# Kernel tuning notes

Measured on AMD Instinct MI355X. Metric: run time of the kernel, lower is better.

## Reference

```python
import jax, jax.numpy as jnp
from jax import lax
import numpy as np

H = 512      # hidden_size
L = 2        # num_layers
IN = 512     # input_size
LAT = 256    # latent_size
B = 256      # batch
S = 256      # seq_length


def setup_inputs() -> dict:
    key = jax.random.key(0)
    ks = jax.random.split(key, 12)
    sd = 0.05
    return {
        "latent": jax.random.normal(ks[0], (B, LAT), dtype=jnp.float32),
        "fc_w": jax.random.normal(ks[1], (H * L * 2, LAT), dtype=jnp.float32) * sd,
        "fc_b": jnp.zeros((H * L * 2,), dtype=jnp.float32),
        "map_w": jax.random.normal(ks[2], (IN, H * 2 * L), dtype=jnp.float32) * sd,
        "map_b": jnp.zeros((IN,), dtype=jnp.float32),
        "wih0": jax.random.normal(ks[3], (4 * H, IN), dtype=jnp.float32) * sd,
        "whh0": jax.random.normal(ks[4], (4 * H, H), dtype=jnp.float32) * sd,
        "bih0": jnp.zeros((4 * H,), dtype=jnp.float32),
        "bhh0": jnp.zeros((4 * H,), dtype=jnp.float32),
        "wih1": jax.random.normal(ks[5], (4 * H, H), dtype=jnp.float32) * sd,
        "whh1": jax.random.normal(ks[6], (4 * H, H), dtype=jnp.float32) * sd,
        "bih1": jnp.zeros((4 * H,), dtype=jnp.float32),
        "bhh1": jnp.zeros((4 * H,), dtype=jnp.float32),
        "seq_length": S,
    }


def _lstm_cell(x, h, c, wih, whh, bih, bhh):
    # torch.nn.LSTMCell gate ordering: i, f, g, o
    g = x @ wih.T + bih + h @ whh.T + bhh
    i, f, gg, o = jnp.split(g, 4, axis=-1)
    c2 = jax.nn.sigmoid(f) * c + jax.nn.sigmoid(i) * jnp.tanh(gg)
    h2 = jax.nn.sigmoid(o) * jnp.tanh(c2)
    return h2, c2


def reference(latent, fc_w, fc_b, map_w, map_b,
              wih0, whh0, bih0, bhh0, wih1, whh1, bih1, bhh1, seq_length):
    bsz = latent.shape[0]
    hid = wih0.shape[0] // 4
    nl = 2
    # dec_hidden = tanh(fc(latent)) -> view(num_layers, B, 2H) -> chunk into (h, c)
    dec = jnp.tanh(latent @ fc_w.T + fc_b)            # (B, 2*L*H)
    dec = dec.reshape(nl, bsz, 2 * hid)               # row-major reinterpret, as torch .view
    h0, c0 = dec[..., :hid], dec[..., hid:]           # each (L, B, H)
    wih = (wih0, wih1); whh = (whh0, whh1)
    bih = (bih0, bih1); bhh = (bhh0, bhh1)

    def step(carry, _):
        h, c = carry
        # cat((h,c), -1).view(B, -1) -- faithful raw reshape across (layer, batch)
        fc_in = jnp.concatenate([h, c], axis=-1).reshape(bsz, -1)  # (B, 2*L*H)
        out = jax.nn.sigmoid(fc_in @ map_w.T + map_b)              # (B, IN)
        x = out
        hs, cs = [], []
        for l in range(nl):
            h2, c2 = _lstm_cell(x, h[l], c[l], wih[l], whh[l], bih[l], bhh[l])
            hs.append(h2); cs.append(c2)
            x = h2
        hn = jnp.tanh(jnp.stack(hs))   # activation_rnn
        cn = jnp.tanh(jnp.stack(cs))   # activation_fc
        return (hn, cn), out

    _, outs = lax.scan(step, (h0, c0), None, length=int(seq_length))
    return outs  # (S, B, IN)
```

## Files before the change

### kernel.cpp

```cpp
#include <hip/hip_runtime.h>

#define SEQ 256

#define WL0     0u
#define WL1     2097152u
#define FCT     4194304u
#define OFF_FC  4718592u
#define OFF_XM  5767168u
#define OFF_X0  5898240u
#define OFF_ARR 6029312u

#define S_AS0 0
#define S_WS0 2304
#define S_AS1 4608
#define S_WS1 6912
#define S_RED 9216
#define S_GS  17664
#define S_TOT 18720

__device__ __forceinline__ float sigf(float x){ return 1.0f/(1.0f + __expf(-x)); }
__device__ __forceinline__ float tanhf_(float x){
  float cx = fminf(fmaxf(x, -15.f), 15.f);
  float e = __expf(2.f*cx);
  return (e-1.f)/(e+1.f);
}

__global__ __launch_bounds__(256) void tr_kernel(const float* __restrict__ src,
                                                 float* __restrict__ dst, int R, int C){
  int i = blockIdx.x*256 + threadIdx.x;
  if (i < R*C){ int r = i / C, c = i - r*C; dst[(size_t)c*R + r] = src[i]; }
}

__global__ __launch_bounds__(256) void wprep(const float* __restrict__ wih0,
                                             const float* __restrict__ whh0,
                                             const float* __restrict__ wih1,
                                             const float* __restrict__ whh1,
                                             float* __restrict__ ws){
  const unsigned idx = blockIdx.x*256u + threadIdx.x;
  const unsigned layer = idx >> 21, rem = idx & 2097151u;
  const unsigned c = rem >> 10, k = rem & 1023u;
  const unsigned j = c >> 2, g = c & 3u;
  const float* wih = layer ? wih1 : wih0;
  const float* whh = layer ? whh1 : whh0;
  const float v = (k < 512u) ? wih[(g*512u + j)*512u + k] : whh[(g*512u + j)*512u + (k - 512u)];
  ws[(layer ? WL1 : WL0) + rem] = v;
}

__global__ __launch_bounds__(256) void init2(const float* __restrict__ latent,
                                             const float* __restrict__ fc_b,
                                             float* __restrict__ ws){
  __shared__ float ls[256];
  const int b = blockIdx.x, tid = threadIdx.x;
  if (tid < 32){
    __hip_atomic_store((unsigned*)(ws + OFF_ARR) + b*32 + tid, 0u,
                       __ATOMIC_RELAXED, __HIP_MEMORY_SCOPE_AGENT);
    __hip_atomic_store((unsigned*)(ws + OFF_ARR) + (b+256)*32 + tid, 0u,
                       __ATOMIC_RELAXED, __HIP_MEMORY_SCOPE_AGENT);
  }
  ls[tid] = latent[b*256 + tid];
  __syncthreads();
  const float* fT = ws + FCT;
  for (int nc = 0; nc < 8; ++nc){
    const int n = nc*256 + tid;
    float acc = fc_b[n];
    for (int k = 0; k < 256; ++k) acc += ls[k] * fT[k*2048 + n];
    const float v = tanhf_(acc);
    const unsigned f = (unsigned)b*2048u + (unsigned)n;
    const unsigned l = f >> 18, p = (f >> 10) & 255u, q = f & 1023u;
    ws[OFF_FC + (l*128u + (p>>1))*2048u + (p&1u)*1024u + q] = v;
  }
}

__device__ __forceinline__ void gsync(unsigned* arr, unsigned epoch, int tid, int blk){
  __syncthreads();
  if (tid == 0)
    __hip_atomic_store(arr + (unsigned)blk*32u, epoch,
                       __ATOMIC_RELEASE, __HIP_MEMORY_SCOPE_AGENT);
  if (tid < 64){
    unsigned m;
    do {
      m = 0xFFFFFFFFu;
      #pragma unroll
      for (int q = 0; q < 8; ++q){
        const unsigned v = __hip_atomic_load(arr + (unsigned)(tid + 64*q)*32u,
                                             __ATOMIC_RELAXED, __HIP_MEMORY_SCOPE_AGENT);
        m = v < m ? v : m;
      }
      if (m < epoch) __builtin_amdgcn_s_sleep(2);
    } while (!__all(m >= epoch));
  }
  __syncthreads();
  if (tid == 0) __builtin_amdgcn_fence(__ATOMIC_ACQUIRE, "agent");
  __syncthreads();
}

__device__ __forceinline__ void fma8x4(float acc[8][4], const float4 A0, const float4 A1,
                                       const float4 W0){
  const float a_[8] = {A0.x,A0.y,A0.z,A0.w,A1.x,A1.y,A1.z,A1.w};
  const float w_[4] = {W0.x,W0.y,W0.z,W0.w};
  #pragma unroll
  for (int i=0;i<8;++i)
    #pragma unroll
    for (int j=0;j<4;++j) acc[i][j] = __builtin_fmaf(a_[i], w_[j], acc[i][j]);
}

__device__ __forceinline__ void map_phase(float* sm, const float* __restrict__ FCc,
    const float* __restrict__ map_w, const float* __restrict__ map_b,
    float* __restrict__ XM, float* __restrict__ outp_t, int tid, int r0, int cb)
{
  const int rg = tid & 3;
  const int ng = (tid >> 2) & 1;
  const int kg = tid >> 3;
  const int n0 = cb * 8;
  float acc[8][4];
  #pragma unroll
  for (int i=0;i<8;++i){
    #pragma unroll
    for (int j=0;j<4;++j) acc[i][j]=0.f;
  }
  float4 va[2]; float4 vw;

  auto LOADS = [&](int ch){
    #pragma unroll
    for (int it=0; it<2; ++it){
      const int e = tid + it*256, r = e>>4, kq = e&15;
      va[it] = *(const float4*)&FCc[(unsigned)(r0+r)*2048u + (unsigned)(ch*64 + kq*4)];
    }
    if (tid < 128){ const int n = tid>>4, kq = tid&15;
      vw = *(const float4*)&map_w[(unsigned)(n0+n)*2048u + (unsigned)(ch*64 + kq*4)]; }
  };
  auto STORES = [&](int buf){
    float* A_ = sm + (buf ? S_AS1 : S_AS0);
    float* W_ = sm + (buf ? S_WS1 : S_WS0);
    #pragma unroll
    for (int it=0; it<2; ++it){
      const int e = tid + it*256, r = e>>4, kq = e&15;
      const int col = r ^ ((kq&7)<<2);
      A_[(kq*4+0)*36 + col] = va[it].x;
      A_[(kq*4+1)*36 + col] = va[it].y;
      A_[(kq*4+2)*36 + col] = va[it].z;
      A_[(kq*4+3)*36 + col] = va[it].w;
    }
    if (tid < 128){ const int n = tid>>4, kq = tid&15;
      const int col = n ^ ((kq&7)<<2);
      W_[(kq*4+0)*36 + col] = vw.x;
      W_[(kq*4+1)*36 + col] = vw.y;
      W_[(kq*4+2)*36 + col] = vw.z;
      W_[(kq*4+3)*36 + col] = vw.w; }
  };
  auto COMPUTE = [&](int buf){
    const float* A_ = sm + (buf ? S_AS1 : S_AS0);
    const float* W_ = sm + (buf ? S_WS1 : S_WS0);
    #pragma unroll
    for (int u=0; u<2; ++u){
      const int k = kg*2 + u;
      const int phi = ((k>>2)&7)<<2;
      const int ca0 = (rg*8) ^ phi;
      const float4 a0 = *(const float4*)&A_[k*36 + ca0];
      const float4 a1 = *(const float4*)&A_[k*36 + (ca0^4)];
      const float4 w0 = *(const float4*)&W_[k*36 + ((ng*4) ^ phi)];
      fma8x4(acc, a0, a1, w0);
    }
  };

  LOADS(0); STORES(1);
  __syncthreads();
  #pragma unroll 1
  for (int ch = 0; ch < 32; ++ch){
    const int buf = (ch & 1) ^ 1;
    if (ch+1 < 32) LOADS(ch+1);
    COMPUTE(buf);
    if (ch+1 < 32) STORES(buf^1);
    __syncthreads();
  }
  float* red = sm + S_RED;
  #pragma unroll
  for (int i=0;i<8;++i){
    #pragma unroll
    for (int j=0;j<4;++j) red[tid*33 + i*4 + j] = acc[i][j];
  }
  __syncthreads();
  {
    const int r = tid >> 3, nl = tid & 7;
    float sum = 0.f;
    #pragma unroll
    for (int kk=0;kk<32;++kk)
      sum += red[((r>>3) + 4*(nl>>2) + 8*kk)*33 + (r&7)*4 + (nl&3)];
    const int n = n0 + nl;
    const float v = sigf(sum + map_b[n]);
    const unsigned off = (unsigned)(r0 + r)*512u + (unsigned)n;
    XM[off] = v;
    outp_t[off] = v;
  }
}

__device__ __forceinline__ void lstm_phase(float* sm, const int l,
    const float* __restrict__ WL, const float* __restrict__ xs,
    const float* __restrict__ FCc, float* __restrict__ FCn,
    float* __restrict__ X0, const float* __restrict__ bih, const float* __restrict__ bhh,
    int tid, int r0, int cb)
{
  const int rg = tid & 3;
  const int ng = (tid >> 2) & 7;
  const int kg = tid >> 5;
  const int c0 = cb * 32;
  float acc[8][4];
  #pragma unroll
  for (int i=0;i<8;++i){
    #pragma unroll
    for (int j=0;j<4;++j) acc[i][j]=0.f;
  }
  float4 va[2], vw4[2];

  auto LOADS = [&](int ch){
    if (ch < 8){
      #pragma unroll
      for (int it=0; it<2; ++it){
        const int e = tid + it*256, r = e>>4, kq = e&15;
        va[it] = *(const float4*)&xs[(unsigned)(r0+r)*512u + (unsigned)(ch*64 + kq*4)];
      }
    } else {
      #pragma unroll
      for (int it=0; it<2; ++it){
        const int e = tid + it*256, r = e>>4, kq = e&15;
        const int b = r0 + r;
        const unsigned q = (unsigned)((ch-8)*64 + kq*4);
        va[it] = *(const float4*)&FCc[(unsigned)((l<<7) + (b>>1))*2048u + (unsigned)(b&1)*1024u + q];
      }
    }
    #pragma unroll
    for (int it=0; it<2; ++it){
      const int e = tid + it*256, n = e>>4, kq = e&15;
      vw4[it] = *(const float4*)&WL[(unsigned)(c0+n)*1024u + (unsigned)(ch*64 + kq*4)];
    }
  };
  auto STORES = [&](int buf){
    float* A_ = sm + (buf ? S_AS1 : S_AS0);
    float* W_ = sm + (buf ? S_WS1 : S_WS0);
    #pragma unroll
    for (int it=0; it<2; ++it){
      const int e = tid + it*256, r = e>>4, kq = e&15;
      const int col = r ^ ((kq&7)<<2);
      A_[(kq*4+0)*36 + col] = va[it].x;
      A_[(kq*4+1)*36 + col] = va[it].y;
      A_[(kq*4+2)*36 + col] = va[it].z;
      A_[(kq*4+3)*36 + col] = va[it].w;
    }
    #pragma unroll
    for (int it=0; it<2; ++it){
      const int e = tid + it*256, n = e>>4, kq = e&15;
      const int col = n ^ ((kq&7)<<2);
      W_[(kq*4+0)*36 + col] = vw4[it].x;
      W_[(kq*4+1)*36 + col] = vw4[it].y;
      W_[(kq*4+2)*36 + col] = vw4[it].z;
      W_[(kq*4+3)*36 + col] = vw4[it].w;
    }
  };
  auto COMPUTE = [&](int buf){
    const float* A_ = sm + (buf ? S_AS1 : S_AS0);
    const float* W_ = sm + (buf ? S_WS1 : S_WS0);
    #pragma unroll
    for (int u=0; u<8; ++u){
      const int k = kg*8 + u;
      const int phi = ((k>>2)&7)<<2;
      const int ca0 = (rg*8) ^ phi;
      const float4 a0 = *(const float4*)&A_[k*36 + ca0];
      const float4 a1 = *(const float4*)&A_[k*36 + (ca0^4)];
      const float4 w0 = *(const float4*)&W_[k*36 + ((ng*4) ^ phi)];
      fma8x4(acc, a0, a1, w0);
    }
  };

  LOADS(0); STORES(1);
  __syncthreads();
  #pragma unroll 1
  for (int ch = 0; ch < 16; ++ch){
    const int buf = (ch & 1) ^ 1;
    if (ch+1 < 16) LOADS(ch+1);
    COMPUTE(buf);
    if (ch+1 < 16) STORES(buf^1);
    __syncthreads();
  }

  float* red = sm + S_RED;
  float* gs  = sm + S_GS;
  #pragma unroll
  for (int i=0;i<8;++i){
    #pragma unroll
    for (int j=0;j<4;++j) red[tid*33 + i*4 + j] = acc[i][j];
  }
  __syncthreads();
  #pragma unroll
  for (int s=0;s<4;++s){
    const int o = tid + s*256;
    const int r = o >> 5, c = o & 31;
    float sum = 0.f;
    #pragma unroll
    for (int kk=0;kk<8;++kk)
      sum += red[((r>>3) + 4*(c>>2) + 32*kk)*33 + (r&7)*4 + (c&3)];
    gs[c*33 + r] = sum;
  }
  __syncthreads();
  const int r = tid & 31, j0 = tid >> 5;
  const int row = r0 + r;
  const unsigned srow = (unsigned)((l<<7) + (row>>1))*2048u + (unsigned)(row&1)*1024u;
  const int jg = cb*8 + j0;
  const float gi = gs[(j0*4+0)*33 + r] + bih[jg]       + bhh[jg];
  const float gf = gs[(j0*4+1)*33 + r] + bih[512+jg]   + bhh[512+jg];
  const float gg = gs[(j0*4+2)*33 + r] + bih[1024+jg]  + bhh[1024+jg];
  const float go = gs[(j0*4+3)*33 + r] + bih[1536+jg]  + bhh[1536+jg];
  const float cp = FCc[srow + 512u + (unsigned)jg];
  const float c2 = sigf(gf)*cp + sigf(gi)*tanhf_(gg);
  const float h2 = sigf(go)*tanhf_(c2);
  if (l == 0) X0[(unsigned)row*512u + (unsigned)jg] = h2;
  FCn[srow + (unsigned)jg]        = tanhf_(h2);
  FCn[srow + 512u + (unsigned)jg] = tanhf_(c2);
}

__launch_bounds__(256, 2)
__global__ void persist(const float* __restrict__ map_w, const float* __restrict__ map_b,
                        const float* __restrict__ bih0, const float* __restrict__ bhh0,
                        const float* __restrict__ bih1, const float* __restrict__ bhh1,
                        float* __restrict__ ws, float* __restrict__ outp)
{
  __shared__ float sm[S_TOT];
  const int tid = threadIdx.x;
  const int blk = blockIdx.x;
  const int cbl = blk & 63;
  const int cb = ((cbl & 7) << 3) | (cbl >> 3);
  const int rb = blk >> 6;
  const int r0 = rb * 32;
  float* FC = ws + OFF_FC;
  float* XM = ws + OFF_XM;
  float* X0 = ws + OFF_X0;
  unsigned* arr = (unsigned*)(ws + OFF_ARR);
  unsigned nsync = 0;

  #pragma unroll 1
  for (int t = 0; t < SEQ; ++t){
    const unsigned cur = (unsigned)(t & 1);
    const float* FCc = FC + cur*524288u;
    float* FCn = FC + (cur^1u)*524288u;

    map_phase(sm, FCc, map_w, map_b, XM, outp + (size_t)t*131072u, tid, r0, cb);
    if (t == SEQ-1) break;
    gsync(arr, ++nsync, tid, blk);
    lstm_phase(sm, 0, ws + WL0, XM, FCc, FCn, X0, bih0, bhh0, tid, r0, cb);
    gsync(arr, ++nsync, tid, blk);
    lstm_phase(sm, 1, ws + WL1, X0, FCc, FCn, X0, bih1, bhh1, tid, r0, cb);
    gsync(arr, ++nsync, tid, blk);
  }
}

extern "C" void kernel_launch(void* const* d_in, const int* in_sizes, int n_in,
                              void* d_out, int out_size, void* d_ws, size_t ws_size,
                              hipStream_t stream)
{
  (void)in_sizes; (void)n_in; (void)out_size; (void)ws_size;
  const float* latent = (const float*)d_in[0];
  const float* fc_w   = (const float*)d_in[1];
  const float* fc_b   = (const float*)d_in[2];
  const float* map_w  = (const float*)d_in[3];
  const float* map_b  = (const float*)d_in[4];
  const float* wih0   = (const float*)d_in[5];
  const float* whh0   = (const float*)d_in[6];
  const float* bih0   = (const float*)d_in[7];
  const float* bhh0   = (const float*)d_in[8];
  const float* wih1   = (const float*)d_in[9];
  const float* whh1   = (const float*)d_in[10];
  const float* bih1   = (const float*)d_in[11];
  const float* bhh1   = (const float*)d_in[12];
  float* ws = (float*)d_ws;
  float* outp = (float*)d_out;

  tr_kernel<<<2048,256,0,stream>>>(fc_w, ws + FCT, 2048, 256);
  wprep<<<16384,256,0,stream>>>(wih0, whh0, wih1, whh1, ws);
  init2<<<256,256,0,stream>>>(latent, fc_b, ws);

  void* args[8];
  args[0] = (void*)&map_w; args[1] = (void*)&map_b;
  args[2] = (void*)&bih0;  args[3] = (void*)&bhh0;
  args[4] = (void*)&bih1;  args[5] = (void*)&bhh1;
  args[6] = (void*)&ws;    args[7] = (void*)&outp;
  hipError_t e = hipLaunchCooperativeKernel((const void*)persist, dim3(512), dim3(256),
                                            args, 0, stream);
  if (e != hipSuccess){
    persist<<<dim3(512), dim3(256), 0, stream>>>(map_w, map_b, bih0, bhh0,
                                                 bih1, bhh1, ws, outp);
  }
}
```

Baseline: 32.81 ms.

## Halve per-block row tile and double persistent grid to 1024 blocks

Each block of the persistent cooperative kernel now handles 16 batch rows instead of 32. The grid doubles to 1024 blocks, with launch bounds raised to 4 blocks per SM and shared memory shrunk by aliasing the reduction buffer over the staging tiles. The aim is more parallelism and occupancy for the per-step GEMMs. In exchange, the grid barrier has twice as many participants to poll, each block reloads the same weight tiles, and per-thread register reuse drops from an 8x4 to a 4x4 micro-tile.

```diff
diff --git a/kernel.cpp b/kernel.cpp
--- a/kernel.cpp
+++ b/kernel.cpp
@@ -14,9 +14,9 @@
 #define S_WS0 2304
 #define S_AS1 4608
 #define S_WS1 6912
-#define S_RED 9216
-#define S_GS  17664
-#define S_TOT 18720
+#define S_RED 0
+#define S_GS  9216
+#define S_TOT 9760
 
 __device__ __forceinline__ float sigf(float x){ return 1.0f/(1.0f + __expf(-x)); }
 __device__ __forceinline__ float tanhf_(float x){
@@ -52,10 +52,10 @@
   __shared__ float ls[256];
   const int b = blockIdx.x, tid = threadIdx.x;
   if (tid < 32){
-    __hip_atomic_store((unsigned*)(ws + OFF_ARR) + b*32 + tid, 0u,
-                       __ATOMIC_RELAXED, __HIP_MEMORY_SCOPE_AGENT);
-    __hip_atomic_store((unsigned*)(ws + OFF_ARR) + (b+256)*32 + tid, 0u,
-                       __ATOMIC_RELAXED, __HIP_MEMORY_SCOPE_AGENT);
+    #pragma unroll
+    for (int s = 0; s < 4; ++s)
+      __hip_atomic_store((unsigned*)(ws + OFF_ARR) + (b + 256*s)*32 + tid, 0u,
+                         __ATOMIC_RELAXED, __HIP_MEMORY_SCOPE_AGENT);
   }
   ls[tid] = latent[b*256 + tid];
   __syncthreads();
@@ -81,7 +81,7 @@
     do {
       m = 0xFFFFFFFFu;
       #pragma unroll
-      for (int q = 0; q < 8; ++q){
+      for (int q = 0; q < 16; ++q){
         const unsigned v = __hip_atomic_load(arr + (unsigned)(tid + 64*q)*32u,
                                              __ATOMIC_RELAXED, __HIP_MEMORY_SCOPE_AGENT);
         m = v < m ? v : m;
@@ -94,12 +94,11 @@
   __syncthreads();
 }
 
-__device__ __forceinline__ void fma8x4(float acc[8][4], const float4 A0, const float4 A1,
-                                       const float4 W0){
-  const float a_[8] = {A0.x,A0.y,A0.z,A0.w,A1.x,A1.y,A1.z,A1.w};
+__device__ __forceinline__ void fma4x4(float acc[4][4], const float4 A0, const float4 W0){
+  const float a_[4] = {A0.x,A0.y,A0.z,A0.w};
   const float w_[4] = {W0.x,W0.y,W0.z,W0.w};
   #pragma unroll
-  for (int i=0;i<8;++i)
+  for (int i=0;i<4;++i)
     #pragma unroll
     for (int j=0;j<4;++j) acc[i][j] = __builtin_fmaf(a_[i], w_[j], acc[i][j]);
 }
@@ -112,35 +111,29 @@
   const int ng = (tid >> 2) & 1;
   const int kg = tid >> 3;
   const int n0 = cb * 8;
-  float acc[8][4];
-  #pragma unroll
-  for (int i=0;i<8;++i){
+  float acc[4][4];
+  #pragma unroll
+  for (int i=0;i<4;++i){
     #pragma unroll
     for (int j=0;j<4;++j) acc[i][j]=0.f;
   }
-  float4 va[2]; float4 vw;
+  float4 va; float4 vw;
 
   auto LOADS = [&](int ch){
-    #pragma unroll
-    for (int it=0; it<2; ++it){
-      const int e = tid + it*256, r = e>>4, kq = e&15;
-      va[it] = *(const float4*)&FCc[(unsigned)(r0+r)*2048u + (unsigned)(ch*64 + kq*4)];
-    }
+    { const int r = tid>>4, kq = tid&15;
+      va = *(const float4*)&FCc[(unsigned)(r0+r)*2048u + (unsigned)(ch*64 + kq*4)]; }
     if (tid < 128){ const int n = tid>>4, kq = tid&15;
       vw = *(const float4*)&map_w[(unsigned)(n0+n)*2048u + (unsigned)(ch*64 + kq*4)]; }
   };
   auto STORES = [&](int buf){
     float* A_ = sm + (buf ? S_AS1 : S_AS0);
     float* W_ = sm + (buf ? S_WS1 : S_WS0);
-    #pragma unroll
-    for (int it=0; it<2; ++it){
-      const int e = tid + it*256, r = e>>4, kq = e&15;
+    { const int r = tid>>4, kq = tid&15;
       const int col = r ^ ((kq&7)<<2);
-      A_[(kq*4+0)*36 + col] = va[it].x;
-      A_[(kq*4+1)*36 + col] = va[it].y;
-      A_[(kq*4+2)*36 + col] = va[it].z;
-      A_[(kq*4+3)*36 + col] = va[it].w;
-    }
+      A_[(kq*4+0)*36 + col] = va.x;
+      A_[(kq*4+1)*36 + col] = va.y;
+      A_[(kq*4+2)*36 + col] = va.z;
+      A_[(kq*4+3)*36 + col] = va.w; }
     if (tid < 128){ const int n = tid>>4, kq = tid&15;
       const int col = n ^ ((kq&7)<<2);
       W_[(kq*4+0)*36 + col] = vw.x;
@@ -155,11 +148,9 @@
     for (int u=0; u<2; ++u){
       const int k = kg*2 + u;
       const int phi = ((k>>2)&7)<<2;
-      const int ca0 = (rg*8) ^ phi;
-      const float4 a0 = *(const float4*)&A_[k*36 + ca0];
-      const float4 a1 = *(const float4*)&A_[k*36 + (ca0^4)];
+      const float4 a0 = *(const float4*)&A_[k*36 + ((rg*4) ^ phi)];
       const float4 w0 = *(const float4*)&W_[k*36 + ((ng*4) ^ phi)];
-      fma8x4(acc, a0, a1, w0);
+      fma4x4(acc, a0, w0);
     }
   };
 
@@ -175,17 +166,17 @@
   }
   float* red = sm + S_RED;
   #pragma unroll
-  for (int i=0;i<8;++i){
-    #pragma unroll
-    for (int j=0;j<4;++j) red[tid*33 + i*4 + j] = acc[i][j];
-  }
-  __syncthreads();
-  {
+  for (int i=0;i<4;++i){
+    #pragma unroll
+    for (int j=0;j<4;++j) red[tid*17 + i*4 + j] = acc[i][j];
+  }
+  __syncthreads();
+  if (tid < 128){
     const int r = tid >> 3, nl = tid & 7;
     float sum = 0.f;
     #pragma unroll
     for (int kk=0;kk<32;++kk)
-      sum += red[((r>>3) + 4*(nl>>2) + 8*kk)*33 + (r&7)*4 + (nl&3)];
+      sum += red[(kk*8 + (nl>>2)*4 + (r>>2))*17 + (r&3)*4 + (nl&3)];
     const int n = n0 + nl;
     const float v = sigf(sum + map_b[n]);
     const unsigned off = (unsigned)(r0 + r)*512u + (unsigned)n;
@@ -204,29 +195,23 @@
   const int ng = (tid >> 2) & 7;
   const int kg = tid >> 5;
   const int c0 = cb * 32;
-  float acc[8][4];
-  #pragma unroll
-  for (int i=0;i<8;++i){
+  float acc[4][4];
+  #pragma unroll
+  for (int i=0;i<4;++i){
     #pragma unroll
     for (int j=0;j<4;++j) acc[i][j]=0.f;
   }
-  float4 va[2], vw4[2];
+  float4 va; float4 vw4[2];
 
   auto LOADS = [&](int ch){
     if (ch < 8){
-      #pragma unroll
-      for (int it=0; it<2; ++it){
-        const int e = tid + it*256, r = e>>4, kq = e&15;
-        va[it] = *(const float4*)&xs[(unsigned)(r0+r)*512u + (unsigned)(ch*64 + kq*4)];
-      }
+      const int r = tid>>4, kq = tid&15;
+      va = *(const float4*)&xs[(unsigned)(r0+r)*512u + (unsigned)(ch*64 + kq*4)];
     } else {
-      #pragma unroll
-      for (int it=0; it<2; ++it){
-        const int e = tid + it*256, r = e>>4, kq = e&15;
-        const int b = r0 + r;
-        const unsigned q = (unsigned)((ch-8)*64 + kq*4);
-        va[it] = *(const float4*)&FCc[(unsigned)((l<<7) + (b>>1))*2048u + (unsigned)(b&1)*1024u + q];
-      }
+      const int r = tid>>4, kq = tid&15;
+      const int b = r0 + r;
+      const unsigned q = (unsigned)((ch-8)*64 + kq*4);
+      va = *(const float4*)&FCc[(unsigned)((l<<7) + (b>>1))*2048u + (unsigned)(b&1)*1024u + q];
     }
     #pragma unroll
     for (int it=0; it<2; ++it){
@@ -237,15 +222,12 @@
   auto STORES = [&](int buf){
     float* A_ = sm + (buf ? S_AS1 : S_AS0);
     float* W_ = sm + (buf ? S_WS1 : S_WS0);
-    #pragma unroll
-    for (int it=0; it<2; ++it){
-      const int e = tid + it*256, r = e>>4, kq = e&15;
+    { const int r = tid>>4, kq = tid&15;
       const int col = r ^ ((kq&7)<<2);
-      A_[(kq*4+0)*36 + col] = va[it].x;
-      A_[(kq*4+1)*36 + col] = va[it].y;
-      A_[(kq*4+2)*36 + col] = va[it].z;
-      A_[(kq*4+3)*36 + col] = va[it].w;
-    }
+      A_[(kq*4+0)*36 + col] = va.x;
+      A_[(kq*4+1)*36 + col] = va.y;
+      A_[(kq*4+2)*36 + col] = va.z;
+      A_[(kq*4+3)*36 + col] = va.w; }
     #pragma unroll
     for (int it=0; it<2; ++it){
       const int e = tid + it*256, n = e>>4, kq = e&15;
@@ -263,11 +245,9 @@
     for (int u=0; u<8; ++u){
       const int k = kg*8 + u;
       const int phi = ((k>>2)&7)<<2;
-      const int ca0 = (rg*8) ^ phi;
-      const float4 a0 = *(const float4*)&A_[k*36 + ca0];
-      const float4 a1 = *(const float4*)&A_[k*36 + (ca0^4)];
+      const float4 a0 = *(const float4*)&A_[k*36 + ((rg*4) ^ phi)];
       const float4 w0 = *(const float4*)&W_[k*36 + ((ng*4) ^ phi)];
-      fma8x4(acc, a0, a1, w0);
+      fma4x4(acc, a0, w0);
     }
   };
 
@@ -285,39 +265,41 @@
   float* red = sm + S_RED;
   float* gs  = sm + S_GS;
   #pragma unroll
-  for (int i=0;i<8;++i){
-    #pragma unroll
-    for (int j=0;j<4;++j) red[tid*33 + i*4 + j] = acc[i][j];
-  }
-  __syncthreads();
-  #pragma unroll
-  for (int s=0;s<4;++s){
+  for (int i=0;i<4;++i){
+    #pragma unroll
+    for (int j=0;j<4;++j) red[tid*17 + i*4 + j] = acc[i][j];
+  }
+  __syncthreads();
+  #pragma unroll
+  for (int s=0;s<2;++s){
     const int o = tid + s*256;
     const int r = o >> 5, c = o & 31;
     float sum = 0.f;
     #pragma unroll
     for (int kk=0;kk<8;++kk)
-      sum += red[((r>>3) + 4*(c>>2) + 32*kk)*33 + (r&7)*4 + (c&3)];
-    gs[c*33 + r] = sum;
-  }
-  __syncthreads();
-  const int r = tid & 31, j0 = tid >> 5;
-  const int row = r0 + r;
-  const unsigned srow = (unsigned)((l<<7) + (row>>1))*2048u + (unsigned)(row&1)*1024u;
-  const int jg = cb*8 + j0;
-  const float gi = gs[(j0*4+0)*33 + r] + bih[jg]       + bhh[jg];
-  const float gf = gs[(j0*4+1)*33 + r] + bih[512+jg]   + bhh[512+jg];
-  const float gg = gs[(j0*4+2)*33 + r] + bih[1024+jg]  + bhh[1024+jg];
-  const float go = gs[(j0*4+3)*33 + r] + bih[1536+jg]  + bhh[1536+jg];
-  const float cp = FCc[srow + 512u + (unsigned)jg];
-  const float c2 = sigf(gf)*cp + sigf(gi)*tanhf_(gg);
-  const float h2 = sigf(go)*tanhf_(c2);
-  if (l == 0) X0[(unsigned)row*512u + (unsigned)jg] = h2;
-  FCn[srow + (unsigned)jg]        = tanhf_(h2);
-  FCn[srow + 512u + (unsigned)jg] = tanhf_(c2);
-}
-
-__launch_bounds__(256, 2)
+      sum += red[(kk*32 + (c>>2)*4 + (r>>2))*17 + (r&3)*4 + (c&3)];
+    gs[c*17 + r] = sum;
+  }
+  __syncthreads();
+  if (tid < 128){
+    const int r = tid & 15, j0 = tid >> 4;
+    const int row = r0 + r;
+    const unsigned srow = (unsigned)((l<<7) + (row>>1))*2048u + (unsigned)(row&1)*1024u;
+    const int jg = cb*8 + j0;
+    const float gi = gs[(j0*4+0)*17 + r] + bih[jg]       + bhh[jg];
+    const float gf = gs[(j0*4+1)*17 + r] + bih[512+jg]   + bhh[512+jg];
+    const float gg = gs[(j0*4+2)*17 + r] + bih[1024+jg]  + bhh[1024+jg];
+    const float go = gs[(j0*4+3)*17 + r] + bih[1536+jg]  + bhh[1536+jg];
+    const float cp = FCc[srow + 512u + (unsigned)jg];
+    const float c2 = sigf(gf)*cp + sigf(gi)*tanhf_(gg);
+    const float h2 = sigf(go)*tanhf_(c2);
+    if (l == 0) X0[(unsigned)row*512u + (unsigned)jg] = h2;
+    FCn[srow + (unsigned)jg]        = tanhf_(h2);
+    FCn[srow + 512u + (unsigned)jg] = tanhf_(c2);
+  }
+}
+
+__launch_bounds__(256, 4)
 __global__ void persist(const float* __restrict__ map_w, const float* __restrict__ map_b,
                         const float* __restrict__ bih0, const float* __restrict__ bhh0,
                         const float* __restrict__ bih1, const float* __restrict__ bhh1,
@@ -329,7 +311,7 @@
   const int cbl = blk & 63;
   const int cb = ((cbl & 7) << 3) | (cbl >> 3);
   const int rb = blk >> 6;
-  const int r0 = rb * 32;
+  const int r0 = rb * 16;
   float* FC = ws + OFF_FC;
   float* XM = ws + OFF_XM;
   float* X0 = ws + OFF_X0;
@@ -382,10 +364,10 @@
   args[2] = (void*)&bih0;  args[3] = (void*)&bhh0;
   args[4] = (void*)&bih1;  args[5] = (void*)&bhh1;
   args[6] = (void*)&ws;    args[7] = (void*)&outp;
-  hipError_t e = hipLaunchCooperativeKernel((const void*)persist, dim3(512), dim3(256),
+  hipError_t e = hipLaunchCooperativeKernel((const void*)persist, dim3(1024), dim3(256),
                                             args, 0, stream);
   if (e != hipSuccess){
-    persist<<<dim3(512), dim3(256), 0, stream>>>(map_w, map_b, bih0, bhh0,
-                                                 bih1, bhh1, ws, outp);
-  }
-}
+    persist<<<dim3(1024), dim3(256), 0, stream>>>(map_w, map_b, bih0, bhh0,
+                                                  bih1, bhh1, ws, outp);
+  }
+}
```

Result: slower. 54.34 ms (+65.6%).
